# Kernel tuning notes

Hardware: AMD Instinct MI355X
Metric: run time of the kernel (lower is better)

The kernel has to match this reference:

```python
import jax, jax.numpy as jnp
import numpy as np

N = 2048      # nodes: 8 sequences x 256 tokens
E = 524288    # edges: dense attention graph, 8 * 256^2
H = 8         # heads
DK = 64       # per-head dim


def setup_inputs() -> dict:
    key = jax.random.key(0)
    k1, k2, k3, k4, k5 = jax.random.split(key, 5)
    q = jax.random.normal(k1, (N, H, DK), dtype=jnp.float32)
    k = jax.random.normal(k2, (N, H, DK), dtype=jnp.float32)
    v = jax.random.normal(k3, (N, H, DK), dtype=jnp.float32)
    edge_src = jax.random.randint(k4, (E,), 0, N, dtype=jnp.int32)
    edge_dst = jax.random.randint(k5, (E,), 0, N, dtype=jnp.int32)
    return {"q": q, "k": k, "v": v, "edge_src": edge_src, "edge_dst": edge_dst}


def reference(q, k, v, edge_src, edge_dst):
    # src_dot_dst('k','q','score'): per-edge dot product over head dim -> [E, H]
    score = jnp.einsum('ehd,ehd->eh', k[edge_src], q[edge_dst])
    # scaled_exp('score', sqrt(d_k)): exp(clamp(score / sqrt(d_k), -10, 10))
    score = jnp.exp(jnp.clip(score / jnp.sqrt(jnp.float32(DK)), -10.0, 10.0))
    # send_and_recv: wv = sum_dst(v_src * score), z = sum_dst(score)
    wv = jax.ops.segment_sum(v[edge_src] * score[:, :, None], edge_dst, num_segments=N)  # [N, H, DK]
    z = jax.ops.segment_sum(score, edge_dst, num_segments=N)  # [N, H]
    # post_func normalization: attention output per node
    return wv / z[:, :, None]
```

## Files before the change

kernel.cpp:

```cpp
#include <hip/hip_runtime.h>

#define NNODES 2048
#define NHEAD 8
#define DKDIM 64

typedef unsigned int uint;
typedef unsigned short ushort;
typedef unsigned char uchar;
typedef __fp16 h2 __attribute__((ext_vector_type(2)));
typedef __fp16 h8 __attribute__((ext_vector_type(8)));
typedef float f4 __attribute__((ext_vector_type(4)));

#define KSCALE 0.18033688011112042f
#define CLAMP2 14.426950408889634f

__device__ __forceinline__ uint pk2(float a, float b) {
    union { h2 h; uint u; } x; x.h = __builtin_amdgcn_cvt_pkrtz(a, b); return x.u;
}

__global__ void conv_k(const float* __restrict__ k, uint4* __restrict__ kc,
                       uint4* __restrict__ A4) {
    int i = blockIdx.x * 256 + threadIdx.x;
    int dim8 = i & 7, node = (i >> 3) & 2047, h = i >> 14;
    const float* src = k + (size_t)node * 512 + h * 64 + dim8 * 8;
    float4 f0 = *(const float4*)src;
    float4 f1 = *(const float4*)(src + 4);
    uint4 o;
    o.x = pk2(f0.x * KSCALE, f0.y * KSCALE);
    o.y = pk2(f0.z * KSCALE, f0.w * KSCALE);
    o.z = pk2(f1.x * KSCALE, f1.y * KSCALE);
    o.w = pk2(f1.z * KSCALE, f1.w * KSCALE);
    kc[(h * 2048 + node) * 8 + dim8] = o;
    uint4 zz = {0u, 0u, 0u, 0u};
    A4[i] = zz;
    A4[i + 131072] = zz;
}

__global__ void conv_vT(const float* __restrict__ v, ushort* __restrict__ vt) {
    __shared__ float tile[64][65];
    int b = blockIdx.x;
    int h = b & 7, tn = b >> 3;
    int t = threadIdx.x;
    int nl = t >> 2, dq = (t & 3) * 16;
    const float* src = v + ((size_t)(tn * 64 + nl)) * 512 + h * 64 + dq;
#pragma unroll
    for (int i = 0; i < 4; ++i) {
        float4 f = *(const float4*)(src + i * 4);
        tile[nl][dq + i * 4 + 0] = f.x;
        tile[nl][dq + i * 4 + 1] = f.y;
        tile[nl][dq + i * 4 + 2] = f.z;
        tile[nl][dq + i * 4 + 3] = f.w;
    }
    __syncthreads();
    int dim = t >> 2, nq = (t & 3) * 16;
    uint wv[8];
#pragma unroll
    for (int i = 0; i < 8; ++i)
        wv[i] = pk2(tile[nq + 2 * i][dim], tile[nq + 2 * i + 1][dim]);
    char* base = (char*)vt + ((size_t)(h * 64 + dim) * 2048 + tn * 64) * 2;
    int nb0 = (t & 3) * 2;
    uint4 lo = { wv[0], wv[1], wv[2], wv[3] };
    uint4 hi = { wv[4], wv[5], wv[6], wv[7] };
    *(uint4*)(base + nb0 * 16) = lo;
    *(uint4*)(base + nb0 * 16 + 16) = hi;
}

__global__ void histA(const int* __restrict__ es, const int* __restrict__ ed,
                      uint* __restrict__ A32, int E) {
    int i = blockIdx.x * 256 + threadIdx.x;
    if (i < E) {
        uint idx = (uint)es[i] * 2048u + (uint)ed[i];
        atomicAdd(&A32[idx >> 2], 1u << ((idx & 3) * 8));
    }
}

__global__ void __launch_bounds__(512, 1) attn_kernel(
    const float* __restrict__ q, const ushort* __restrict__ kc, const ushort* __restrict__ vt,
    const uchar* __restrict__ A8, float* __restrict__ out) {
    __shared__ __align__(16) char LK[2][2][8192];
    __shared__ __align__(16) char LV[2][2][8192];
    __shared__ __align__(16) char LA[2][2][4096];
    __shared__ __align__(16) char LS[8][2304];

    int b = blockIdx.x;
    int h = b & 7;
    int dst0 = (b >> 3) * 64;
    int t = threadIdx.x;
    int w = t >> 6, half = w >> 2, wq = w & 3;
    int l = t & 63, c = l & 15, g = l >> 4;
    int ht = t & 255;

    const char* kH = (const char*)kc + (size_t)h * 262144;
    const char* vH = (const char*)vt + (size_t)h * 262144;

    h8 qf[2];
    {
        const float* qp = q + (size_t)(dst0 + wq * 16 + c) * 512 + h * 64 + g * 8;
#pragma unroll
        for (int ch = 0; ch < 2; ++ch) {
            float4 f0 = *(const float4*)(qp + ch * 32);
            float4 f1 = *(const float4*)(qp + ch * 32 + 4);
            union { uint u[4]; h8 v; } U;
            U.u[0] = pk2(f0.x, f0.y); U.u[1] = pk2(f0.z, f0.w);
            U.u[2] = pk2(f1.x, f1.y); U.u[3] = pk2(f1.z, f1.w);
            qf[ch] = U.v;
        }
    }

    f4 of[4];
#pragma unroll
    for (int i = 0; i < 4; ++i) of[i] = (f4){0.f, 0.f, 0.f, 0.f};
    float z = 0.f;

    int r0 = ht >> 3, b0 = ht & 7;
    int ar_ = ht >> 2, as_ = ht & 3;
    uint4 kr[2], vr[2], ar;
    int ts0 = half * 16;

#pragma unroll
    for (int j = 0; j < 2; ++j) {
        int row = r0 + j * 32;
        kr[j] = *(const uint4*)(kH + (size_t)(ts0 * 64 + row) * 128 + b0 * 16);
        vr[j] = *(const uint4*)(vH + (size_t)row * 4096 + ts0 * 128 + b0 * 16);
        *(uint4*)(LK[half][0] + row * 128 + b0 * 16) = kr[j];
        *(uint4*)(LV[half][0] + row * 128 + b0 * 16) = vr[j];
    }
    ar = *(const uint4*)(A8 + (size_t)(ts0 * 64 + ar_) * 2048 + dst0 + as_ * 16);
    *(uint4*)(LA[half][0] + ar_ * 64 + as_ * 16) = ar;
    __syncthreads();

    for (int it = 0; it < 16; ++it) {
        int cur = it & 1;
        int ts = ts0 + it;
        if (it < 15) {
#pragma unroll
            for (int j = 0; j < 2; ++j) {
                int row = r0 + j * 32;
                kr[j] = *(const uint4*)(kH + (size_t)((ts + 1) * 64 + row) * 128 + b0 * 16);
                vr[j] = *(const uint4*)(vH + (size_t)row * 4096 + (ts + 1) * 128 + b0 * 16);
            }
            ar = *(const uint4*)(A8 + (size_t)((ts + 1) * 64 + ar_) * 2048 + dst0 + as_ * 16);
        }

        f4 sacc[4];
#pragma unroll
        for (int i = 0; i < 4; ++i) sacc[i] = (f4){0.f, 0.f, 0.f, 0.f};
#pragma unroll
        for (int nt = 0; nt < 4; ++nt)
#pragma unroll
            for (int ch = 0; ch < 2; ++ch) {
                h8 kf = *(const h8*)(LK[half][cur] + (nt * 16 + c) * 128 + (ch * 4 + g) * 16);
                sacc[nt] = __builtin_amdgcn_mfma_f32_16x16x32_f16(kf, qf[ch], sacc[nt], 0, 0, 0);
            }

        char* Sw = LS[w];
        const uchar* Ac = (const uchar*)LA[half][cur];
#pragma unroll
        for (int nt = 0; nt < 4; ++nt)
#pragma unroll
            for (int r = 0; r < 4; ++r) {
                float sc = fminf(fmaxf(sacc[nt][r], -CLAMP2), CLAMP2);
                float m = (float)Ac[(nt * 16 + 4 * g + r) * 64 + wq * 16 + c];
                float e = exp2f(sc) * m;
                z += e;
                *(ushort*)(Sw + c * 144 + (nt * 16 + 4 * g + r) * 2) = (ushort)pk2(e, e);
            }
        asm volatile("" ::: "memory");

        h8 sf[2];
#pragma unroll
        for (int ch = 0; ch < 2; ++ch)
            sf[ch] = *(const h8*)(Sw + c * 144 + (ch * 32 + 8 * g) * 2);
#pragma unroll
        for (int nt = 0; nt < 4; ++nt)
#pragma unroll
            for (int ch = 0; ch < 2; ++ch) {
                h8 vf = *(const h8*)(LV[half][cur] + (nt * 16 + c) * 128 + (ch * 4 + g) * 16);
                of[nt] = __builtin_amdgcn_mfma_f32_16x16x32_f16(vf, sf[ch], of[nt], 0, 0, 0);
            }

        if (it < 15) {
            int nb = cur ^ 1;
#pragma unroll
            for (int j = 0; j < 2; ++j) {
                int row = r0 + j * 32;
                *(uint4*)(LK[half][nb] + row * 128 + b0 * 16) = kr[j];
                *(uint4*)(LV[half][nb] + row * 128 + b0 * 16) = vr[j];
            }
            *(uint4*)(LA[half][nb] + ar_ * 64 + as_ * 16) = ar;
        }
        __syncthreads();
    }

    z += __shfl_xor(z, 16);
    z += __shfl_xor(z, 32);

    float* CL = (float*)&LK[0][0][0];
    float* CLz = (float*)&LV[0][0][0];
    if (half == 1) {
#pragma unroll
        for (int nt = 0; nt < 4; ++nt)
#pragma unroll
            for (int r = 0; r < 4; ++r)
                CL[(wq * 16 + c) * 65 + nt * 16 + 4 * g + r] = of[nt][r];
        if (l < 16) CLz[wq * 16 + c] = z;
    }
    __syncthreads();
    if (half == 0) {
        float zt = 1.0f / (z + CLz[wq * 16 + c]);
#pragma unroll
        for (int nt = 0; nt < 4; ++nt)
#pragma unroll
            for (int r = 0; r < 4; ++r) {
                int idx = (wq * 16 + c) * 65 + nt * 16 + 4 * g + r;
                CL[idx] = (of[nt][r] + CL[idx]) * zt;
            }
    }
    __syncthreads();
#pragma unroll
    for (int j = 0; j < 8; ++j) {
        int i2 = w * 8 + j;
        out[(size_t)(dst0 + i2) * 512 + h * 64 + l] = CL[i2 * 65 + l];
    }
}


extern "C" void kernel_launch(void* const* d_in, const int* in_sizes, int n_in,
                              void* d_out, int out_size, void* d_ws, size_t ws_size,
                              hipStream_t stream) {
    const float* q = (const float*)d_in[0];
    const float* k = (const float*)d_in[1];
    const float* v = (const float*)d_in[2];
    const int* esrc = (const int*)d_in[3];
    const int* edst = (const int*)d_in[4];
    float* out = (float*)d_out;
    const int E = in_sizes[3];

    uchar* A8 = (uchar*)d_ws;
    ushort* kc = (ushort*)(A8 + (size_t)NNODES * NNODES);
    ushort* vt = kc + (size_t)NHEAD * NNODES * DKDIM;

    conv_k<<<512, 256, 0, stream>>>(k, (uint4*)kc, (uint4*)A8);
    conv_vT<<<256, 256, 0, stream>>>(v, vt);
    histA<<<(E + 255) / 256, 256, 0, stream>>>(esrc, edst, (uint*)A8, E);
    attn_kernel<<<256, 512, 0, stream>>>(q, kc, vt, A8, out);
}
```

Before: 69.28 us.

## Split source range across 1024 blocks with partial outputs and combine kernel

The attention kernel now splits the 2048 source nodes into four quarters, each handled by its own 256-thread block, giving 1024 blocks instead of 256 blocks of two halves. Partial weighted sums and normalisers go to workspace, and a new combine kernel adds them and normalises. The score-to-operand transpose now uses lane shuffles instead of an LDS staging buffer. This is meant to raise occupancy and the number of CUs in use, at the cost of an extra launch and a round trip of partial results through global memory.

New measurement: 76.21 us. 1.1x slower.

```diff
diff --git a/kernel.cpp b/kernel.cpp
--- a/kernel.cpp
+++ b/kernel.cpp
@@ -74,28 +74,24 @@
     }
 }
 
-__global__ void __launch_bounds__(512, 1) attn_kernel(
+__global__ void __launch_bounds__(256, 4) attn_kernel(
     const float* __restrict__ q, const ushort* __restrict__ kc, const ushort* __restrict__ vt,
-    const uchar* __restrict__ A8, float* __restrict__ out) {
-    __shared__ __align__(16) char LK[2][2][8192];
-    __shared__ __align__(16) char LV[2][2][8192];
-    __shared__ __align__(16) char LA[2][2][4096];
-    __shared__ __align__(16) char LS[8][2304];
+    const uchar* __restrict__ A8, float* __restrict__ po, float* __restrict__ pz) {
+    __shared__ __align__(16) char LK[2][8192];
+    __shared__ __align__(16) char LV[2][8192];
+    __shared__ __align__(16) char LA[2][4096];
 
     int b = blockIdx.x;
-    int h = b & 7;
-    int dst0 = (b >> 3) * 64;
-    int t = threadIdx.x;
-    int w = t >> 6, half = w >> 2, wq = w & 3;
-    int l = t & 63, c = l & 15, g = l >> 4;
-    int ht = t & 255;
+    int sq = b >> 8, bh = b & 255;
+    int h = bh & 7, dst0 = (bh >> 3) * 64;
+    int t = threadIdx.x, w = t >> 6, l = t & 63, c = l & 15, g = l >> 4;
 
     const char* kH = (const char*)kc + (size_t)h * 262144;
     const char* vH = (const char*)vt + (size_t)h * 262144;
 
     h8 qf[2];
     {
-        const float* qp = q + (size_t)(dst0 + wq * 16 + c) * 512 + h * 64 + g * 8;
+        const float* qp = q + (size_t)(dst0 + w * 16 + c) * 512 + h * 64 + g * 8;
 #pragma unroll
         for (int ch = 0; ch < 2; ++ch) {
             float4 f0 = *(const float4*)(qp + ch * 32);
@@ -112,34 +108,37 @@
     for (int i = 0; i < 4; ++i) of[i] = (f4){0.f, 0.f, 0.f, 0.f};
     float z = 0.f;
 
-    int r0 = ht >> 3, b0 = ht & 7;
-    int ar_ = ht >> 2, as_ = ht & 3;
+    int r0 = t >> 3, b0 = t & 7;
+    int ar_ = t >> 2, as_ = t & 3;
+    int gts0 = sq * 8;
     uint4 kr[2], vr[2], ar;
-    int ts0 = half * 16;
 
 #pragma unroll
     for (int j = 0; j < 2; ++j) {
         int row = r0 + j * 32;
-        kr[j] = *(const uint4*)(kH + (size_t)(ts0 * 64 + row) * 128 + b0 * 16);
-        vr[j] = *(const uint4*)(vH + (size_t)row * 4096 + ts0 * 128 + b0 * 16);
-        *(uint4*)(LK[half][0] + row * 128 + b0 * 16) = kr[j];
-        *(uint4*)(LV[half][0] + row * 128 + b0 * 16) = vr[j];
-    }
-    ar = *(const uint4*)(A8 + (size_t)(ts0 * 64 + ar_) * 2048 + dst0 + as_ * 16);
-    *(uint4*)(LA[half][0] + ar_ * 64 + as_ * 16) = ar;
+        kr[j] = *(const uint4*)(kH + (size_t)(gts0 * 64 + row) * 128 + b0 * 16);
+        vr[j] = *(const uint4*)(vH + (size_t)row * 4096 + gts0 * 128 + b0 * 16);
+        *(uint4*)(LK[0] + row * 128 + b0 * 16) = kr[j];
+        *(uint4*)(LV[0] + row * 128 + b0 * 16) = vr[j];
+    }
+    ar = *(const uint4*)(A8 + (size_t)(gts0 * 64 + ar_) * 2048 + dst0 + as_ * 16);
+    *(uint4*)(LA[0] + ar_ * 64 + as_ * 16) = ar;
     __syncthreads();
 
-    for (int it = 0; it < 16; ++it) {
+    int sl = c + 32 * (g & 1);
+    bool hi = (g >> 1) != 0;
+
+    for (int it = 0; it < 8; ++it) {
         int cur = it & 1;
-        int ts = ts0 + it;
-        if (it < 15) {
+        int gts = gts0 + it;
+        if (it < 7) {
 #pragma unroll
             for (int j = 0; j < 2; ++j) {
                 int row = r0 + j * 32;
-                kr[j] = *(const uint4*)(kH + (size_t)((ts + 1) * 64 + row) * 128 + b0 * 16);
-                vr[j] = *(const uint4*)(vH + (size_t)row * 4096 + (ts + 1) * 128 + b0 * 16);
-            }
-            ar = *(const uint4*)(A8 + (size_t)((ts + 1) * 64 + ar_) * 2048 + dst0 + as_ * 16);
+                kr[j] = *(const uint4*)(kH + (size_t)((gts + 1) * 64 + row) * 128 + b0 * 16);
+                vr[j] = *(const uint4*)(vH + (size_t)row * 4096 + (gts + 1) * 128 + b0 * 16);
+            }
+            ar = *(const uint4*)(A8 + (size_t)((gts + 1) * 64 + ar_) * 2048 + dst0 + as_ * 16);
         }
 
         f4 sacc[4];
@@ -149,45 +148,60 @@
         for (int nt = 0; nt < 4; ++nt)
 #pragma unroll
             for (int ch = 0; ch < 2; ++ch) {
-                h8 kf = *(const h8*)(LK[half][cur] + (nt * 16 + c) * 128 + (ch * 4 + g) * 16);
+                h8 kf = *(const h8*)(LK[cur] + (nt * 16 + c) * 128 + (ch * 4 + g) * 16);
                 sacc[nt] = __builtin_amdgcn_mfma_f32_16x16x32_f16(kf, qf[ch], sacc[nt], 0, 0, 0);
             }
 
-        char* Sw = LS[w];
-        const uchar* Ac = (const uchar*)LA[half][cur];
+        uint pw[4][2];
+        {
+            const uchar* Ac = (const uchar*)LA[cur];
+#pragma unroll
+            for (int nt = 0; nt < 4; ++nt) {
+                float e[4];
+#pragma unroll
+                for (int r = 0; r < 4; ++r) {
+                    float sc = fminf(fmaxf(sacc[nt][r], -CLAMP2), CLAMP2);
+                    float m = (float)Ac[(nt * 16 + 4 * g + r) * 64 + w * 16 + c];
+                    e[r] = exp2f(sc) * m;
+                    z += e[r];
+                }
+                pw[nt][0] = pk2(e[0], e[1]);
+                pw[nt][1] = pk2(e[2], e[3]);
+            }
+        }
+
+        h8 sf[2];
+#pragma unroll
+        for (int ch = 0; ch < 2; ++ch) {
+            uint a0 = __shfl(pw[2 * ch][0], sl),      b0_ = __shfl(pw[2 * ch + 1][0], sl);
+            uint a1 = __shfl(pw[2 * ch][1], sl),      b1_ = __shfl(pw[2 * ch + 1][1], sl);
+            uint a2 = __shfl(pw[2 * ch][0], sl + 16), b2_ = __shfl(pw[2 * ch + 1][0], sl + 16);
+            uint a3 = __shfl(pw[2 * ch][1], sl + 16), b3_ = __shfl(pw[2 * ch + 1][1], sl + 16);
+            union { uint u[4]; h8 v; } S;
+            S.u[0] = hi ? b0_ : a0;
+            S.u[1] = hi ? b1_ : a1;
+            S.u[2] = hi ? b2_ : a2;
+            S.u[3] = hi ? b3_ : a3;
+            sf[ch] = S.v;
+        }
+
 #pragma unroll
         for (int nt = 0; nt < 4; ++nt)
 #pragma unroll
-            for (int r = 0; r < 4; ++r) {
-                float sc = fminf(fmaxf(sacc[nt][r], -CLAMP2), CLAMP2);
-                float m = (float)Ac[(nt * 16 + 4 * g + r) * 64 + wq * 16 + c];
-                float e = exp2f(sc) * m;
-                z += e;
-                *(ushort*)(Sw + c * 144 + (nt * 16 + 4 * g + r) * 2) = (ushort)pk2(e, e);
-            }
-        asm volatile("" ::: "memory");
-
-        h8 sf[2];
-#pragma unroll
-        for (int ch = 0; ch < 2; ++ch)
-            sf[ch] = *(const h8*)(Sw + c * 144 + (ch * 32 + 8 * g) * 2);
-#pragma unroll
-        for (int nt = 0; nt < 4; ++nt)
-#pragma unroll
             for (int ch = 0; ch < 2; ++ch) {
-                h8 vf = *(const h8*)(LV[half][cur] + (nt * 16 + c) * 128 + (ch * 4 + g) * 16);
+                h8 vf = *(const h8*)(LV[cur] + (nt * 16 + c) * 128 + (ch * 4 + g) * 16);
                 of[nt] = __builtin_amdgcn_mfma_f32_16x16x32_f16(vf, sf[ch], of[nt], 0, 0, 0);
             }
 
-        if (it < 15) {
+        if (it < 7) {
             int nb = cur ^ 1;
 #pragma unroll
             for (int j = 0; j < 2; ++j) {
                 int row = r0 + j * 32;
-                *(uint4*)(LK[half][nb] + row * 128 + b0 * 16) = kr[j];
-                *(uint4*)(LV[half][nb] + row * 128 + b0 * 16) = vr[j];
-            }
-            *(uint4*)(LA[half][nb] + ar_ * 64 + as_ * 16) = ar;
+                *(uint4*)(LK[nb] + row * 128 + b0 * 16) = kr[j];
+                *(uint4*)(LV[nb] + row * 128 + b0 * 16) = vr[j];
+            }
+            *(uint4*)(LA[nb] + ar_ * 64 + as_ * 16) = ar;
         }
         __syncthreads();
     }
@@ -195,32 +209,38 @@
     z += __shfl_xor(z, 16);
     z += __shfl_xor(z, 32);
 
-    float* CL = (float*)&LK[0][0][0];
-    float* CLz = (float*)&LV[0][0][0];
-    if (half == 1) {
-#pragma unroll
-        for (int nt = 0; nt < 4; ++nt)
-#pragma unroll
-            for (int r = 0; r < 4; ++r)
-                CL[(wq * 16 + c) * 65 + nt * 16 + 4 * g + r] = of[nt][r];
-        if (l < 16) CLz[wq * 16 + c] = z;
-    }
-    __syncthreads();
-    if (half == 0) {
-        float zt = 1.0f / (z + CLz[wq * 16 + c]);
-#pragma unroll
-        for (int nt = 0; nt < 4; ++nt)
-#pragma unroll
-            for (int r = 0; r < 4; ++r) {
-                int idx = (wq * 16 + c) * 65 + nt * 16 + 4 * g + r;
-                CL[idx] = (of[nt][r] + CL[idx]) * zt;
-            }
-    }
-    __syncthreads();
-#pragma unroll
-    for (int j = 0; j < 8; ++j) {
-        int i2 = w * 8 + j;
-        out[(size_t)(dst0 + i2) * 512 + h * 64 + l] = CL[i2 * 65 + l];
+#pragma unroll
+    for (int nt = 0; nt < 4; ++nt) {
+        float4 o4 = { of[nt][0], of[nt][1], of[nt][2], of[nt][3] };
+        *(float4*)&po[(size_t)b * 4096 + (w * 16 + c) * 64 + nt * 16 + 4 * g] = o4;
+    }
+    if (l < 16) pz[(size_t)b * 64 + w * 16 + c] = z;
+}
+
+__global__ void combine_kernel(const float* __restrict__ po, const float* __restrict__ pz,
+                               float* __restrict__ out) {
+    int cb = blockIdx.x;
+    int h = cb & 7, dt = cb >> 3;
+    int t = threadIdx.x, dl = t >> 2, dq = (t & 3) * 16;
+    float4 acc[4] = {{0.f,0.f,0.f,0.f},{0.f,0.f,0.f,0.f},{0.f,0.f,0.f,0.f},{0.f,0.f,0.f,0.f}};
+    float zs = 0.f;
+#pragma unroll
+    for (int sq = 0; sq < 4; ++sq) {
+        const float4* P = (const float4*)(po + (size_t)(sq * 256 + cb) * 4096 + dl * 64 + dq);
+#pragma unroll
+        for (int i = 0; i < 4; ++i) {
+            float4 x = P[i];
+            acc[i].x += x.x; acc[i].y += x.y; acc[i].z += x.z; acc[i].w += x.w;
+        }
+        zs += pz[(size_t)(sq * 256 + cb) * 64 + dl];
+    }
+    float inv = 1.0f / zs;
+    float4* O = (float4*)(out + (size_t)(dt * 64 + dl) * 512 + h * 64 + dq);
+#pragma unroll
+    for (int i = 0; i < 4; ++i) {
+        float4 x = acc[i];
+        x.x *= inv; x.y *= inv; x.z *= inv; x.w *= inv;
+        O[i] = x;
     }
 }
 
@@ -239,9 +259,12 @@
     uchar* A8 = (uchar*)d_ws;
     ushort* kc = (ushort*)(A8 + (size_t)NNODES * NNODES);
     ushort* vt = kc + (size_t)NHEAD * NNODES * DKDIM;
+    float* po = (float*)(vt + (size_t)NHEAD * NNODES * DKDIM);
+    float* pz = po + (size_t)1024 * 4096;
 
     conv_k<<<512, 256, 0, stream>>>(k, (uint4*)kc, (uint4*)A8);
     conv_vT<<<256, 256, 0, stream>>>(v, vt);
     histA<<<(E + 255) / 256, 256, 0, stream>>>(esrc, edst, (uint*)A8, E);
-    attn_kernel<<<256, 512, 0, stream>>>(q, kc, vt, A8, out);
-}
+    attn_kernel<<<1024, 256, 0, stream>>>(q, kc, vt, A8, po, pz);
+    combine_kernel<<<256, 256, 0, stream>>>(po, pz, out);
+}
```
